# Optimization experiments

Hardware: AMD Instinct MI355X
Metric: run time of the kernel (lower is better)

Reference implementation:

```python
import jax, jax.numpy as jnp
import numpy as np

NEG_SLOPE_GAT = 0.2   # PyG GATConv default negative_slope
NEG_SLOPE = 0.01      # torch.nn.LeakyReLU default
NUM_AISLES = 20       # aisle_nrs drawn from [0,20); matches aisle_nrs.max()+1


def leaky(x, s):
    return jnp.where(x >= 0, x, s * x)


def gat_conv(x, src, dst, W, a_src, a_dst, b, n_nodes):
    """Single-head PyG GATConv (self-loops already appended to src/dst)."""
    h = x @ W                                        # [N, C]
    es = h @ a_src                                   # [N]
    ed = h @ a_dst                                   # [N]
    e = leaky(es[src] + ed[dst], NEG_SLOPE_GAT)      # [E] per-edge score
    m = jax.ops.segment_max(e, dst, num_segments=n_nodes)
    w = jnp.exp(e - m[dst])
    z = jax.ops.segment_sum(w, dst, num_segments=n_nodes)
    alpha = w / z[dst]                               # segment softmax over incoming edges
    out = jax.ops.segment_sum(h[src] * alpha[:, None], dst, num_segments=n_nodes)
    return out + b


def setup_inputs() -> dict:
    key = jax.random.key(0)
    ks = jax.random.split(key, 32)
    B, N, E = 16, 2048, 32768
    Fin, H, O, HA = 32, 128, 64, 256

    def glorot(k, shape):
        fan = shape[0] + shape[-1]
        return jax.random.uniform(k, shape, jnp.float32, -1.0, 1.0) * np.sqrt(6.0 / fan)

    inp = {
        "graph_nodes": jax.random.normal(ks[0], (B, N, Fin), jnp.float32),
        "aisle_nrs": jax.random.randint(ks[1], (B, N), 0, NUM_AISLES),
        "graph_edge_links": jax.random.randint(ks[2], (B, 2, E), 0, N),
        "mask": jax.random.randint(ks[3], (B, N), 0, 2),
        "picks_left": jax.random.randint(ks[4], (B,), 0, 100),
        # GAT layer 1: Fin -> H
        "W1": glorot(ks[5], (Fin, H)), "as1": glorot(ks[6], (H,)), "ad1": glorot(ks[7], (H,)), "b1": jnp.zeros((H,), jnp.float32),
        # GAT layer 2: H -> H
        "W2": glorot(ks[8], (H, H)), "as2": glorot(ks[9], (H,)), "ad2": glorot(ks[10], (H,)), "b2": jnp.zeros((H,), jnp.float32),
        # GAT layer 3: H -> O
        "W3": glorot(ks[11], (H, O)), "as3": glorot(ks[12], (O,)), "ad3": glorot(ks[13], (O,)), "b3": jnp.zeros((O,), jnp.float32),
        # post-embedding MLP head
        "lw1": glorot(ks[14], (2 * O, HA)), "lb1": jnp.zeros((HA,), jnp.float32),
        "lw2": glorot(ks[15], (HA, O)), "lb2": jnp.zeros((O,), jnp.float32),
        "lw3": glorot(ks[16], (O, 1)), "lb3": jnp.zeros((1,), jnp.float32),
    }
    return inp


def reference(graph_nodes, aisle_nrs, graph_edge_links, mask, picks_left,
              W1, as1, ad1, b1, W2, as2, ad2, b2, W3, as3, ad3, b3,
              lw1, lb1, lw2, lb2, lw3, lb3):
    B, N, Fin = graph_nodes.shape
    NT = B * N
    x = graph_nodes.reshape(NT, Fin)

    # batch the graphs: offset per-graph edge indices, append self-loops
    off = (jnp.arange(B) * N)[:, None]
    src = (graph_edge_links[:, 0, :] + off).reshape(-1)
    dst = (graph_edge_links[:, 1, :] + off).reshape(-1)
    loops = jnp.arange(NT)
    src = jnp.concatenate([src, loops])
    dst = jnp.concatenate([dst, loops])

    x = gat_conv(x, src, dst, W1, as1, ad1, b1, NT)
    x = gat_conv(x, src, dst, W2, as2, ad2, b2, NT)
    x = gat_conv(x, src, dst, W3, as3, ad3, b3, NT)

    # scatter-mean aisle embedding
    batch_idx = jnp.repeat(jnp.arange(B), N)
    aid = aisle_nrs.reshape(-1) + batch_idx * NUM_AISLES   # [NT]
    S = B * NUM_AISLES
    ssum = jax.ops.segment_sum(x, aid, num_segments=S)
    cnt = jax.ops.segment_sum(jnp.ones((NT,), x.dtype), aid, num_segments=S)
    emb = ssum / jnp.maximum(cnt, 1.0)[:, None]

    x = jnp.concatenate([x, emb[aid]], axis=1)             # [NT, 2*O]
    x = leaky(x @ lw1 + lb1, NEG_SLOPE)
    x = leaky(x @ lw2 + lb2, NEG_SLOPE)
    x = (x @ lw3 + lb3).reshape(B, N)

    logits = jnp.where(mask != 0, x, -jnp.inf)
    return jax.nn.softmax(logits, axis=1)
```

## Files before the change

### kernel.cpp

```cpp
#include <hip/hip_runtime.h>
#include <hip/hip_bf16.h>
#include <math.h>
#include <stdint.h>

#define BATCH 16
#define NNODE 2048
#define EPG   32768
#define NT    (BATCH * NNODE)
#define ET    (BATCH * EPG + NT)
#define NUM_AISLES 20
#define SEG   (BATCH * NUM_AISLES)
#define NEG_GAT 0.2f
#define NEG_MLP 0.01f
#define ACHUNK 8
#define CAP 64

typedef __attribute__((ext_vector_type(8))) short s16x8;
typedef __attribute__((ext_vector_type(4))) float f32x4;

__device__ __forceinline__ void split_bf16(float v, unsigned short& hi, unsigned short& lo) {
    unsigned int u = __float_as_uint(v);
    unsigned int r = u + 0x7FFFu + ((u >> 16) & 1u);
    hi = (unsigned short)(r >> 16);
    float fh = __uint_as_float(((unsigned int)hi) << 16);
    float rem = v - fh;
    unsigned int u2 = __float_as_uint(rem);
    unsigned int r2 = u2 + 0x7FFFu + ((u2 >> 16) & 1u);
    lo = (unsigned short)(r2 >> 16);
}

template <int K, int KC, int NOUT, int COLS>
__device__ __forceinline__ void prep_one(const float* __restrict__ W,
                                         unsigned short* __restrict__ dst, int idx) {
    constexpr int SWM = (KC >= 64) ? 7 : 3;
    int k = idx / NOUT, col = idx - k * NOUT;
    int ch = k / KC, kl = k - ch * KC;
    int ct = col / COLS, n = col - ct * COLS;
    int tile = ct * (K / KC) + ch;
    unsigned short h, l;
    split_bf16(W[idx], h, l);
    size_t base = (size_t)tile * (2 * COLS * KC);
    int pos = n * KC + (kl ^ ((n & SWM) << 3));
    dst[base + pos] = h;
    dst[base + COLS * KC + pos] = l;
}

__global__ __launch_bounds__(256) void prep_weights(const float* __restrict__ W1,
                                                    const float* __restrict__ W2,
                                                    const float* __restrict__ W3,
                                                    const float* __restrict__ lw1,
                                                    const float* __restrict__ lw2,
                                                    unsigned short* __restrict__ P1,
                                                    unsigned short* __restrict__ P2,
                                                    unsigned short* __restrict__ P3,
                                                    unsigned short* __restrict__ P4,
                                                    unsigned short* __restrict__ P5) {
    int b = blockIdx.x, t = threadIdx.x;
    if (b < 16)        prep_one<32, 32, 128, 128>(W1, P1, b * 256 + t);
    else if (b < 80)   prep_one<128, 64, 128, 128>(W2, P2, (b - 16) * 256 + t);
    else if (b < 112)  prep_one<128, 128, 64, 64>(W3, P3, (b - 80) * 256 + t);
    else if (b < 240)  prep_one<128, 64, 256, 128>(lw1, P4, (b - 112) * 256 + t);
    else               prep_one<256, 128, 64, 64>(lw2, P5, (b - 240) * 256 + t);
}

__global__ __launch_bounds__(256) void edge_scatter(const int* __restrict__ links,
                                                    int* __restrict__ cnt,
                                                    int* __restrict__ col_bkt) {
    int b = blockIdx.x;
    int s, d;
    if (b < 2048) {
        int xcd = b & 7, idx = b >> 3;
        int g = xcd * 2 + (idx >> 7);
        int chunk = idx & 127;
        int i = chunk * 256 + threadIdx.x;
        const int* pb = links + (size_t)g * 2 * EPG;
        s = pb[i] + (g << 11);
        d = pb[EPG + i] + (g << 11);
    } else {
        int b2 = b - 2048;
        int xcd = b2 & 7, idx = b2 >> 3;
        int g = xcd * 2 + (idx >> 3);
        int chunk = idx & 7;
        s = d = g * NNODE + chunk * 256 + threadIdx.x;
    }
    int pos = atomicAdd(&cnt[d], 1);
    if (pos < CAP) col_bkt[d * CAP + pos] = s;
}

template <int K, int KC, int NOUT, int COLS, bool LEAKY, bool ATTN, bool FINAL, bool CONCAT>
__global__ __launch_bounds__(256) void gemm_mfma(const float* __restrict__ A,
                                                 const unsigned short* __restrict__ WP,
                                                 const float* __restrict__ bias,
                                                 float* __restrict__ out,
                                                 const float* __restrict__ a_src,
                                                 const float* __restrict__ a_dst,
                                                 float* __restrict__ es,
                                                 float* __restrict__ ed,
                                                 const float* __restrict__ emb,
                                                 const int* __restrict__ aisle,
                                                 const float* __restrict__ lw3,
                                                 const float* __restrict__ lb3,
                                                 const int* __restrict__ mask,
                                                 float* __restrict__ logits) {
    constexpr int C = COLS / 16;
    constexpr int SWM = (KC >= 64) ? 7 : 3;
    constexpr int TILE_US = COLS * KC;
    constexpr int TB2 = 2 * TILE_US * 2;
    static_assert(TB2 % 4096 == 0, "chunk must be a multiple of one 256-thread 16B sweep");

    __shared__ unsigned short WS[2 * TILE_US];

    const int tid = threadIdx.x;
    const int wave = tid >> 6, lane = tid & 63;
    const int quad = lane >> 4, l15 = lane & 15;
    const int row0 = blockIdx.x * 64;
    const int m = row0 + wave * 16 + l15;

    f32x4 acc[C];
#pragma unroll
    for (int c = 0; c < C; ++c)
#pragma unroll
        for (int v = 0; v < 4; ++v) acc[c][v] = 0.f;

    union SU { s16x8 v; unsigned short u[8]; };

    for (int kb = 0; kb < K; kb += KC) {
        const char* gsrc = (const char*)WP
            + (size_t)(blockIdx.y * (K / KC) + kb / KC) * TB2;
#pragma unroll
        for (int s = 0; s < TB2 / 4096; ++s) {
            __builtin_amdgcn_global_load_lds(
                (const __attribute__((address_space(1))) void*)(gsrc + s * 4096 + wave * 1024 + lane * 16),
                (__attribute__((address_space(3))) void*)&WS[(s * 4096 + wave * 1024) >> 1],
                16, 0, 0);
        }
        __syncthreads();

        for (int kc = kb; kc < kb + KC; kc += 32) {
            const int off = kc + quad * 8;
            const float* srcp;
            if constexpr (CONCAT) {
                if (off < 64) {
                    srcp = A + (size_t)m * 64 + off;
                } else {
                    int g = m >> 11;
                    srcp = emb + ((size_t)(g * NUM_AISLES + aisle[m])) * 64 + (off - 64);
                }
            } else {
                srcp = A + (size_t)m * K + off;
            }
            float4 v0 = ((const float4*)srcp)[0];
            float4 v1 = ((const float4*)srcp)[1];
            float a8[8] = {v0.x, v0.y, v0.z, v0.w, v1.x, v1.y, v1.z, v1.w};
            SU ah, al;
#pragma unroll
            for (int j = 0; j < 8; ++j) split_bf16(a8[j], ah.u[j], al.u[j]);

            const int kq = (kc - kb) + quad * 8;
#pragma unroll
            for (int c = 0; c < C; ++c) {
                int n = c * 16 + l15;
                int pos = n * KC + (kq ^ ((n & SWM) << 3));
                s16x8 wh = *(const s16x8*)&WS[pos];
                s16x8 wl = *(const s16x8*)&WS[TILE_US + pos];
                acc[c] = __builtin_amdgcn_mfma_f32_16x16x32_bf16(ah.v, wh, acc[c], 0, 0, 0);
                acc[c] = __builtin_amdgcn_mfma_f32_16x16x32_bf16(ah.v, wl, acc[c], 0, 0, 0);
                acc[c] = __builtin_amdgcn_mfma_f32_16x16x32_bf16(al.v, wh, acc[c], 0, 0, 0);
            }
        }
        if (kb + KC < K) __syncthreads();
    }
    if constexpr (FINAL) {
#pragma unroll
        for (int reg = 0; reg < 4; ++reg) {
            float p = 0.f;
#pragma unroll
            for (int c = 0; c < C; ++c) {
                int colx = c * 16 + l15;
                float v = acc[c][reg] + bias[colx];
                v = v >= 0.f ? v : NEG_MLP * v;
                p += v * lw3[colx];
            }
#pragma unroll
            for (int mk = 1; mk < 16; mk <<= 1) p += __shfl_xor(p, mk, 64);
            if (l15 == 0) {
                int row = row0 + wave * 16 + quad * 4 + reg;
                float lg = p + lb3[0];
                logits[row] = (mask[row] != 0) ? lg : -INFINITY;
            }
        }
    } else {
#pragma unroll
        for (int c = 0; c < C; ++c) {
            int colx = blockIdx.y * COLS + c * 16 + l15;
            float bv = bias ? bias[colx] : 0.f;
#pragma unroll
            for (int reg = 0; reg < 4; ++reg) {
                int row = row0 + wave * 16 + quad * 4 + reg;
                float v = acc[c][reg] + bv;
                if (LEAKY) v = v >= 0.f ? v : NEG_MLP * v;
                out[(size_t)row * NOUT + colx] = v;
            }
        }
        if constexpr (ATTN) {
#pragma unroll
            for (int reg = 0; reg < 4; ++reg) {
                float ps = 0.f, pd = 0.f;
#pragma unroll
                for (int c = 0; c < C; ++c) {
                    int colx = c * 16 + l15;
                    float v = acc[c][reg];
                    ps += v * a_src[colx];
                    pd += v * a_dst[colx];
                }
#pragma unroll
                for (int mk = 1; mk < 16; mk <<= 1) {
                    ps += __shfl_xor(ps, mk, 64);
                    pd += __shfl_xor(pd, mk, 64);
                }
                if (l15 == 0) {
                    int row = row0 + wave * 16 + quad * 4 + reg;
                    es[row] = ps;
                    ed[row] = pd;
                }
            }
        }
    }
}

template <int HD>
__global__ __launch_bounds__(256) void gat_aggregate(const float* __restrict__ h,
                                                     const float* __restrict__ es,
                                                     const float* __restrict__ ed,
                                                     const int* __restrict__ cnt,
                                                     const int* __restrict__ col_bkt,
                                                     const float* __restrict__ bias,
                                                     float* __restrict__ out) {
    int b = blockIdx.x;
    int xcd = b & 7, q = b >> 3;
    int graph = xcd * 2 + (q >> 9);
    int node = graph * NNODE + (q & 511) * 4 + (threadIdx.x >> 6);
    int lane = threadIdx.x & 63;
    int deg = cnt[node];
    deg = deg < CAP ? deg : CAP;
    float edv = ed[node];

    float e0 = -INFINITY;
    int c0v = 0;
    if (lane < deg) {
        c0v = col_bkt[node * CAP + lane];
        float e = es[c0v] + edv;
        e0 = e >= 0.f ? e : NEG_GAT * e;
    }
    float m = e0;
#pragma unroll
    for (int off = 32; off; off >>= 1) m = fmaxf(m, __shfl_xor(m, off, 64));
    float z = __expf(e0 - m);
#pragma unroll
    for (int off = 32; off; off >>= 1) z += __shfl_xor(z, off, 64);
    float w0 = __expf(e0 - m) / z;

    const int quad = lane >> 4, l15 = lane & 15;
    if (HD == 128) {
        float a0 = 0.f, a1 = 0.f, a2 = 0.f, a3 = 0.f;
        float a4 = 0.f, a5 = 0.f, a6 = 0.f, a7 = 0.f;
        for (int jj = 0; jj < deg; jj += 4) {
            int j2 = jj + quad;
            int s = __shfl(c0v, j2, 64);
            float w = __shfl(w0, j2, 64);
            const float* base = h + (size_t)s * 128 + l15 * 8;
            float4 v0 = *(const float4*)base;
            float4 v1 = *(const float4*)(base + 4);
            a0 += w * v0.x; a1 += w * v0.y; a2 += w * v0.z; a3 += w * v0.w;
            a4 += w * v1.x; a5 += w * v1.y; a6 += w * v1.z; a7 += w * v1.w;
        }
#pragma unroll
        for (int off = 16; off <= 32; off <<= 1) {
            a0 += __shfl_xor(a0, off, 64); a1 += __shfl_xor(a1, off, 64);
            a2 += __shfl_xor(a2, off, 64); a3 += __shfl_xor(a3, off, 64);
            a4 += __shfl_xor(a4, off, 64); a5 += __shfl_xor(a5, off, 64);
            a6 += __shfl_xor(a6, off, 64); a7 += __shfl_xor(a7, off, 64);
        }
        if (quad == 0) {
            const float* bb = bias + l15 * 8;
            float4 o0, o1;
            o0.x = a0 + bb[0]; o0.y = a1 + bb[1]; o0.z = a2 + bb[2]; o0.w = a3 + bb[3];
            o1.x = a4 + bb[4]; o1.y = a5 + bb[5]; o1.z = a6 + bb[6]; o1.w = a7 + bb[7];
            float* op = out + (size_t)node * 128 + l15 * 8;
            *(float4*)op = o0;
            *(float4*)(op + 4) = o1;
        }
    } else {
        float a0 = 0.f, a1 = 0.f, a2 = 0.f, a3 = 0.f;
        for (int jj = 0; jj < deg; jj += 4) {
            int j2 = jj + quad;
            int s = __shfl(c0v, j2, 64);
            float w = __shfl(w0, j2, 64);
            float4 v = *(const float4*)(h + (size_t)s * 64 + l15 * 4);
            a0 += w * v.x; a1 += w * v.y; a2 += w * v.z; a3 += w * v.w;
        }
#pragma unroll
        for (int off = 16; off <= 32; off <<= 1) {
            a0 += __shfl_xor(a0, off, 64); a1 += __shfl_xor(a1, off, 64);
            a2 += __shfl_xor(a2, off, 64); a3 += __shfl_xor(a3, off, 64);
        }
        if (quad == 0) {
            const float* bb = bias + l15 * 4;
            float4 o;
            o.x = a0 + bb[0]; o.y = a1 + bb[1]; o.z = a2 + bb[2]; o.w = a3 + bb[3];
            *(float4*)(out + (size_t)node * 64 + l15 * 4) = o;
        }
    }
}

__global__ __launch_bounds__(256) void aisle_partial(const float* __restrict__ x3,
                                                     const int* __restrict__ aisle,
                                                     float* __restrict__ psum,
                                                     int* __restrict__ pcnt) {
    int g = blockIdx.x >> 3;
    int ch = blockIdx.x & 7;
    int f = threadIdx.x & 63;
    int stripe = threadIdx.x >> 6;

    __shared__ float sacc[4][NUM_AISLES][64];
    __shared__ int scnt[4][NUM_AISLES];
    for (int i = threadIdx.x; i < 4 * NUM_AISLES * 64; i += 256)
        ((float*)sacc)[i] = 0.f;
    for (int i = threadIdx.x; i < 4 * NUM_AISLES; i += 256)
        ((int*)scnt)[i] = 0;
    __syncthreads();

    const int* ai = aisle + g * NNODE;
    const float* xg = x3 + (size_t)g * NNODE * 64;
    int n0 = ch * 256 + stripe * 64;
#pragma unroll 4
    for (int i = 0; i < 64; ++i) {
        int n = n0 + i;
        int a = ai[n];
        float v = xg[(size_t)n * 64 + f];
        sacc[stripe][a][f] += v;
        if (f == 0) scnt[stripe][a]++;
    }
    __syncthreads();

    for (int i = threadIdx.x; i < NUM_AISLES * 64; i += 256) {
        int a = i >> 6, ff = i & 63;
        psum[((size_t)blockIdx.x * NUM_AISLES + a) * 64 + ff] =
            sacc[0][a][ff] + sacc[1][a][ff] + sacc[2][a][ff] + sacc[3][a][ff];
    }
    for (int i = threadIdx.x; i < NUM_AISLES; i += 256) {
        pcnt[blockIdx.x * NUM_AISLES + i] =
            scnt[0][i] + scnt[1][i] + scnt[2][i] + scnt[3][i];
    }
}

__global__ __launch_bounds__(256) void aisle_reduce(const float* __restrict__ psum,
                                                    const int* __restrict__ pcnt,
                                                    float* __restrict__ emb) {
    int idx = blockIdx.x * 256 + threadIdx.x;
    if (idx >= SEG * 64) return;
    int seg = idx >> 6;
    int f = idx & 63;
    int g = seg / NUM_AISLES;
    int a = seg - g * NUM_AISLES;
    float s = 0.f;
    int c = 0;
#pragma unroll
    for (int ch = 0; ch < ACHUNK; ++ch) {
        int blk = g * ACHUNK + ch;
        s += psum[((size_t)blk * NUM_AISLES + a) * 64 + f];
        c += pcnt[blk * NUM_AISLES + a];
    }
    emb[idx] = s / fmaxf((float)c, 1.0f);
}

__global__ __launch_bounds__(256) void softmax_kernel(const float* __restrict__ logits,
                                                      float* __restrict__ out) {
    int b = blockIdx.x;
    const float* lr = logits + b * NNODE;
    __shared__ float red[4], redz[4];
    float m = -INFINITY;
    for (int i = threadIdx.x; i < NNODE; i += 256) m = fmaxf(m, lr[i]);
#pragma unroll
    for (int off = 32; off; off >>= 1) m = fmaxf(m, __shfl_xor(m, off, 64));
    if ((threadIdx.x & 63) == 0) red[threadIdx.x >> 6] = m;
    __syncthreads();
    m = fmaxf(fmaxf(red[0], red[1]), fmaxf(red[2], red[3]));
    float z = 0.f;
    for (int i = threadIdx.x; i < NNODE; i += 256) z += __expf(lr[i] - m);
#pragma unroll
    for (int off = 32; off; off >>= 1) z += __shfl_xor(z, off, 64);
    if ((threadIdx.x & 63) == 0) redz[threadIdx.x >> 6] = z;
    __syncthreads();
    z = redz[0] + redz[1] + redz[2] + redz[3];
    float invz = 1.0f / z;
    for (int i = threadIdx.x; i < NNODE; i += 256) {
        float v = lr[i];
        out[b * NNODE + i] = (v == -INFINITY) ? 0.f : __expf(v - m) * invz;
    }
}


extern "C" void kernel_launch(void* const* d_in, const int* in_sizes, int n_in,
                              void* d_out, int out_size, void* d_ws, size_t ws_size,
                              hipStream_t stream) {
    const float* gn   = (const float*)d_in[0];
    const int* aisle  = (const int*)d_in[1];
    const int* links  = (const int*)d_in[2];
    const int* mask   = (const int*)d_in[3];
    const float* W1  = (const float*)d_in[5];
    const float* as1 = (const float*)d_in[6];
    const float* ad1 = (const float*)d_in[7];
    const float* b1  = (const float*)d_in[8];
    const float* W2  = (const float*)d_in[9];
    const float* as2 = (const float*)d_in[10];
    const float* ad2 = (const float*)d_in[11];
    const float* b2  = (const float*)d_in[12];
    const float* W3  = (const float*)d_in[13];
    const float* as3 = (const float*)d_in[14];
    const float* ad3 = (const float*)d_in[15];
    const float* b3  = (const float*)d_in[16];
    const float* lw1 = (const float*)d_in[17];
    const float* lb1 = (const float*)d_in[18];
    const float* lw2 = (const float*)d_in[19];
    const float* lb2 = (const float*)d_in[20];
    const float* lw3 = (const float*)d_in[21];
    const float* lb3 = (const float*)d_in[22];
    float* out = (float*)d_out;

    float* ws = (float*)d_ws;
    float* h      = ws;
    float* xb     = h + (size_t)NT * 128;
    float* es     = xb + (size_t)NT * 128;
    float* ed     = es + NT;
    float* emb    = ed + NT;
    float* y1     = emb + SEG * 64;
    float* y2     = y1 + (size_t)NT * 256;
    float* logits = y2 + (size_t)NT * 64;
    float* psum   = logits + NT;
    int* pcnt     = (int*)(psum + 128 * NUM_AISLES * 64);
    int* row_ptr  = pcnt + 128 * NUM_AISLES;
    int* cnt      = row_ptr + NT + 1;
    int* col_bkt  = (int*)y2;

    unsigned short* wsplit = (unsigned short*)(((uintptr_t)(cnt + NT) + 255) & ~(uintptr_t)255);
    unsigned short* P1 = wsplit;
    unsigned short* P2 = P1 + 8192;
    unsigned short* P3 = P2 + 32768;
    unsigned short* P4 = P3 + 16384;
    unsigned short* P5 = P4 + 65536;

    const int EB = (ET + 255) / 256;

    hipMemsetAsync(cnt, 0, NT * sizeof(int), stream);
    prep_weights<<<304, 256, 0, stream>>>(W1, W2, W3, lw1, lw2, P1, P2, P3, P4, P5);
    edge_scatter<<<EB, 256, 0, stream>>>(links, cnt, col_bkt);

    gemm_mfma<32, 32, 128, 128, false, true, false, false><<<dim3(NT / 64, 1), 256, 0, stream>>>(
        gn, P1, nullptr, h, as1, ad1, es, ed, nullptr, nullptr, nullptr, nullptr, nullptr, nullptr);
    gat_aggregate<128><<<NT / 4, 256, 0, stream>>>(h, es, ed, cnt, col_bkt, b1, xb);

    gemm_mfma<128, 64, 128, 128, false, true, false, false><<<dim3(NT / 64, 1), 256, 0, stream>>>(
        xb, P2, nullptr, h, as2, ad2, es, ed, nullptr, nullptr, nullptr, nullptr, nullptr, nullptr);
    gat_aggregate<128><<<NT / 4, 256, 0, stream>>>(h, es, ed, cnt, col_bkt, b2, xb);

    gemm_mfma<128, 128, 64, 64, false, true, false, false><<<dim3(NT / 64, 1), 256, 0, stream>>>(
        xb, P3, nullptr, h, as3, ad3, es, ed, nullptr, nullptr, nullptr, nullptr, nullptr, nullptr);
    gat_aggregate<64><<<NT / 4, 256, 0, stream>>>(h, es, ed, cnt, col_bkt, b3, xb);

    aisle_partial<<<BATCH * ACHUNK, 256, 0, stream>>>(xb, aisle, psum, pcnt);
    aisle_reduce<<<(SEG * 64 + 255) / 256, 256, 0, stream>>>(psum, pcnt, emb);

    gemm_mfma<128, 64, 256, 128, true, false, false, true><<<dim3(NT / 64, 2), 256, 0, stream>>>(
        xb, P4, lb1, y1, nullptr, nullptr, nullptr, nullptr, emb, aisle, nullptr, nullptr, nullptr, nullptr);
    gemm_mfma<256, 128, 64, 64, true, false, true, false><<<dim3(NT / 64, 1), 256, 0, stream>>>(
        y1, P5, lb2, y2, nullptr, nullptr, nullptr, nullptr, nullptr, nullptr, lw3, lb3, mask, logits);

    softmax_kernel<<<BATCH, 256, 0, stream>>>(logits, out);
}
```

Baseline: 284.8 us.

## Fuse launches and store activations pre-split as packed bf16 hi/lo pairs

Folds the counter memset into the weight-prep kernel, merges edge scatter with the first GEMM launch, and computes the aisle mean inside the concat GEMM via shared memory instead of a separate reduce kernel. Aggregation and MLP outputs are now stored as packed hi/lo bf16 words, so consuming GEMMs skip the per-element split in their inner loop. This cuts launch count and redundant conversion ALU work. In exchange, the packed representation drops some low mantissa bits, and every concat block recomputes the aisle embedding.

Result: faster. 277.0 us (-2.8%).

```diff
diff --git a/kernel.cpp b/kernel.cpp
--- a/kernel.cpp
+++ b/kernel.cpp
@@ -14,6 +14,7 @@
 #define NEG_MLP 0.01f
 #define ACHUNK 8
 #define CAP 64
+#define EMB_LD 72
 
 typedef __attribute__((ext_vector_type(8))) short s16x8;
 typedef __attribute__((ext_vector_type(4))) float f32x4;
@@ -27,6 +28,16 @@
     unsigned int u2 = __float_as_uint(rem);
     unsigned int r2 = u2 + 0x7FFFu + ((u2 >> 16) & 1u);
     lo = (unsigned short)(r2 >> 16);
+}
+
+__device__ __forceinline__ unsigned int pack_bf16(float v) {
+    unsigned short h, l;
+    split_bf16(v, h, l);
+    return ((unsigned int)h << 16) | l;
+}
+
+__device__ __forceinline__ float unpack_f32(unsigned int u) {
+    return __uint_as_float(u & 0xffff0000u) + __uint_as_float(u << 16);
 }
 
 template <int K, int KC, int NOUT, int COLS>
@@ -54,19 +65,20 @@
                                                     unsigned short* __restrict__ P2,
                                                     unsigned short* __restrict__ P3,
                                                     unsigned short* __restrict__ P4,
-                                                    unsigned short* __restrict__ P5) {
+                                                    unsigned short* __restrict__ P5,
+                                                    int* __restrict__ cnt) {
     int b = blockIdx.x, t = threadIdx.x;
     if (b < 16)        prep_one<32, 32, 128, 128>(W1, P1, b * 256 + t);
     else if (b < 80)   prep_one<128, 64, 128, 128>(W2, P2, (b - 16) * 256 + t);
     else if (b < 112)  prep_one<128, 128, 64, 64>(W3, P3, (b - 80) * 256 + t);
     else if (b < 240)  prep_one<128, 64, 256, 128>(lw1, P4, (b - 112) * 256 + t);
-    else               prep_one<256, 128, 64, 64>(lw2, P5, (b - 240) * 256 + t);
-}
-
-__global__ __launch_bounds__(256) void edge_scatter(const int* __restrict__ links,
-                                                    int* __restrict__ cnt,
-                                                    int* __restrict__ col_bkt) {
-    int b = blockIdx.x;
+    else if (b < 304)  prep_one<256, 128, 64, 64>(lw2, P5, (b - 240) * 256 + t);
+    else               cnt[(b - 304) * 256 + t] = 0;
+}
+
+__device__ __forceinline__ void scatter_body(int b, const int* __restrict__ links,
+                                             int* __restrict__ cnt,
+                                             int* __restrict__ col_bkt) {
     int s, d;
     if (b < 2048) {
         int xcd = b & 7, idx = b >> 3;
@@ -87,21 +99,24 @@
     if (pos < CAP) col_bkt[d * CAP + pos] = s;
 }
 
-template <int K, int KC, int NOUT, int COLS, bool LEAKY, bool ATTN, bool FINAL, bool CONCAT>
-__global__ __launch_bounds__(256) void gemm_mfma(const float* __restrict__ A,
-                                                 const unsigned short* __restrict__ WP,
-                                                 const float* __restrict__ bias,
-                                                 float* __restrict__ out,
-                                                 const float* __restrict__ a_src,
-                                                 const float* __restrict__ a_dst,
-                                                 float* __restrict__ es,
-                                                 float* __restrict__ ed,
-                                                 const float* __restrict__ emb,
-                                                 const int* __restrict__ aisle,
-                                                 const float* __restrict__ lw3,
-                                                 const float* __restrict__ lb3,
-                                                 const int* __restrict__ mask,
-                                                 float* __restrict__ logits) {
+template <int K, int KC, int NOUT, int COLS, bool LEAKY, bool ATTN, bool FINAL,
+          bool CONCAT, bool PACKEDA, bool PACKOUT>
+__device__ __forceinline__ void gemm_body(int bx, int by,
+                                          const void* __restrict__ Aptr,
+                                          const unsigned short* __restrict__ WP,
+                                          const float* __restrict__ bias,
+                                          void* __restrict__ outp,
+                                          const float* __restrict__ a_src,
+                                          const float* __restrict__ a_dst,
+                                          float* __restrict__ es,
+                                          float* __restrict__ ed,
+                                          const float* __restrict__ psum,
+                                          const int* __restrict__ pcnt,
+                                          const int* __restrict__ aisle,
+                                          const float* __restrict__ lw3,
+                                          const float* __restrict__ lb3,
+                                          const int* __restrict__ mask,
+                                          float* __restrict__ logits) {
     constexpr int C = COLS / 16;
     constexpr int SWM = (KC >= 64) ? 7 : 3;
     constexpr int TILE_US = COLS * KC;
@@ -109,12 +124,30 @@
     static_assert(TB2 % 4096 == 0, "chunk must be a multiple of one 256-thread 16B sweep");
 
     __shared__ unsigned short WS[2 * TILE_US];
+    __shared__ float emb_s[CONCAT ? NUM_AISLES * EMB_LD : 1];
 
     const int tid = threadIdx.x;
     const int wave = tid >> 6, lane = tid & 63;
     const int quad = lane >> 4, l15 = lane & 15;
-    const int row0 = blockIdx.x * 64;
+    const int row0 = bx * 64;
     const int m = row0 + wave * 16 + l15;
+
+    int am = 0;
+    if constexpr (CONCAT) {
+        int g = row0 >> 11;
+        for (int i = tid; i < NUM_AISLES * 64; i += 256) {
+            int a = i >> 6, f = i & 63;
+            float s = 0.f;
+            int c = 0;
+#pragma unroll
+            for (int ch = 0; ch < ACHUNK; ++ch) {
+                s += psum[((size_t)(g * ACHUNK + ch) * NUM_AISLES + a) * 64 + f];
+                c += pcnt[(g * ACHUNK + ch) * NUM_AISLES + a];
+            }
+            emb_s[a * EMB_LD + f] = s / fmaxf((float)c, 1.0f);
+        }
+        am = aisle[m];
+    }
 
     f32x4 acc[C];
 #pragma unroll
@@ -126,7 +159,7 @@
 
     for (int kb = 0; kb < K; kb += KC) {
         const char* gsrc = (const char*)WP
-            + (size_t)(blockIdx.y * (K / KC) + kb / KC) * TB2;
+            + (size_t)(by * (K / KC) + kb / KC) * TB2;
 #pragma unroll
         for (int s = 0; s < TB2 / 4096; ++s) {
             __builtin_amdgcn_global_load_lds(
@@ -138,23 +171,44 @@
 
         for (int kc = kb; kc < kb + KC; kc += 32) {
             const int off = kc + quad * 8;
-            const float* srcp;
+            SU ah, al;
             if constexpr (CONCAT) {
                 if (off < 64) {
-                    srcp = A + (size_t)m * 64 + off;
+                    const unsigned int* ap = (const unsigned int*)Aptr + (size_t)m * 64 + off;
+                    uint4 u0 = ((const uint4*)ap)[0];
+                    uint4 u1 = ((const uint4*)ap)[1];
+                    unsigned int uu[8] = {u0.x, u0.y, u0.z, u0.w, u1.x, u1.y, u1.z, u1.w};
+#pragma unroll
+                    for (int j = 0; j < 8; ++j) {
+                        ah.u[j] = (unsigned short)(uu[j] >> 16);
+                        al.u[j] = (unsigned short)uu[j];
+                    }
                 } else {
-                    int g = m >> 11;
-                    srcp = emb + ((size_t)(g * NUM_AISLES + aisle[m])) * 64 + (off - 64);
+                    const float* ep = &emb_s[am * EMB_LD + (off - 64)];
+                    float4 v0 = ((const float4*)ep)[0];
+                    float4 v1 = ((const float4*)ep)[1];
+                    float a8[8] = {v0.x, v0.y, v0.z, v0.w, v1.x, v1.y, v1.z, v1.w};
+#pragma unroll
+                    for (int j = 0; j < 8; ++j) split_bf16(a8[j], ah.u[j], al.u[j]);
+                }
+            } else if constexpr (PACKEDA) {
+                const unsigned int* ap = (const unsigned int*)Aptr + (size_t)m * K + off;
+                uint4 u0 = ((const uint4*)ap)[0];
+                uint4 u1 = ((const uint4*)ap)[1];
+                unsigned int uu[8] = {u0.x, u0.y, u0.z, u0.w, u1.x, u1.y, u1.z, u1.w};
+#pragma unroll
+                for (int j = 0; j < 8; ++j) {
+                    ah.u[j] = (unsigned short)(uu[j] >> 16);
+                    al.u[j] = (unsigned short)uu[j];
                 }
             } else {
-                srcp = A + (size_t)m * K + off;
-            }
-            float4 v0 = ((const float4*)srcp)[0];
-            float4 v1 = ((const float4*)srcp)[1];
-            float a8[8] = {v0.x, v0.y, v0.z, v0.w, v1.x, v1.y, v1.z, v1.w};
-            SU ah, al;
-#pragma unroll
-            for (int j = 0; j < 8; ++j) split_bf16(a8[j], ah.u[j], al.u[j]);
+                const float* srcp = (const float*)Aptr + (size_t)m * K + off;
+                float4 v0 = ((const float4*)srcp)[0];
+                float4 v1 = ((const float4*)srcp)[1];
+                float a8[8] = {v0.x, v0.y, v0.z, v0.w, v1.x, v1.y, v1.z, v1.w};
+#pragma unroll
+                for (int j = 0; j < 8; ++j) split_bf16(a8[j], ah.u[j], al.u[j]);
+            }
 
             const int kq = (kc - kb) + quad * 8;
 #pragma unroll
@@ -192,14 +246,18 @@
     } else {
 #pragma unroll
         for (int c = 0; c < C; ++c) {
-            int colx = blockIdx.y * COLS + c * 16 + l15;
+            int colx = by * COLS + c * 16 + l15;
             float bv = bias ? bias[colx] : 0.f;
 #pragma unroll
             for (int reg = 0; reg < 4; ++reg) {
                 int row = row0 + wave * 16 + quad * 4 + reg;
                 float v = acc[c][reg] + bv;
                 if (LEAKY) v = v >= 0.f ? v : NEG_MLP * v;
-                out[(size_t)row * NOUT + colx] = v;
+                if constexpr (PACKOUT) {
+                    ((unsigned int*)outp)[(size_t)row * NOUT + colx] = pack_bf16(v);
+                } else {
+                    ((float*)outp)[(size_t)row * NOUT + colx] = v;
+                }
             }
         }
         if constexpr (ATTN) {
@@ -228,6 +286,47 @@
     }
 }
 
+template <int K, int KC, int NOUT, int COLS, bool LEAKY, bool ATTN, bool FINAL,
+          bool CONCAT, bool PACKEDA, bool PACKOUT>
+__global__ __launch_bounds__(256) void gemm_mfma(const void* __restrict__ A,
+                                                 const unsigned short* __restrict__ WP,
+                                                 const float* __restrict__ bias,
+                                                 void* __restrict__ out,
+                                                 const float* __restrict__ a_src,
+                                                 const float* __restrict__ a_dst,
+                                                 float* __restrict__ es,
+                                                 float* __restrict__ ed,
+                                                 const float* __restrict__ psum,
+                                                 const int* __restrict__ pcnt,
+                                                 const int* __restrict__ aisle,
+                                                 const float* __restrict__ lw3,
+                                                 const float* __restrict__ lb3,
+                                                 const int* __restrict__ mask,
+                                                 float* __restrict__ logits) {
+    gemm_body<K, KC, NOUT, COLS, LEAKY, ATTN, FINAL, CONCAT, PACKEDA, PACKOUT>(
+        blockIdx.x, blockIdx.y, A, WP, bias, out, a_src, a_dst, es, ed,
+        psum, pcnt, aisle, lw3, lb3, mask, logits);
+}
+
+__global__ __launch_bounds__(256) void gemm1_scatter(const float* __restrict__ A,
+                                                     const unsigned short* __restrict__ WP,
+                                                     float* __restrict__ out,
+                                                     const float* __restrict__ a_src,
+                                                     const float* __restrict__ a_dst,
+                                                     float* __restrict__ es,
+                                                     float* __restrict__ ed,
+                                                     const int* __restrict__ links,
+                                                     int* __restrict__ cnt,
+                                                     int* __restrict__ col_bkt) {
+    if (blockIdx.x >= NT / 64) {
+        scatter_body(blockIdx.x - NT / 64, links, cnt, col_bkt);
+        return;
+    }
+    gemm_body<32, 32, 128, 128, false, true, false, false, false, false>(
+        blockIdx.x, 0, A, WP, nullptr, out, a_src, a_dst, es, ed,
+        nullptr, nullptr, nullptr, nullptr, nullptr, nullptr, nullptr);
+}
+
 template <int HD>
 __global__ __launch_bounds__(256) void gat_aggregate(const float* __restrict__ h,
                                                      const float* __restrict__ es,
@@ -235,7 +334,7 @@
                                                      const int* __restrict__ cnt,
                                                      const int* __restrict__ col_bkt,
                                                      const float* __restrict__ bias,
-                                                     float* __restrict__ out) {
+                                                     unsigned int* __restrict__ out) {
     int b = blockIdx.x;
     int xcd = b & 7, q = b >> 3;
     int graph = xcd * 2 + (q >> 9);
@@ -283,12 +382,14 @@
         }
         if (quad == 0) {
             const float* bb = bias + l15 * 8;
-            float4 o0, o1;
-            o0.x = a0 + bb[0]; o0.y = a1 + bb[1]; o0.z = a2 + bb[2]; o0.w = a3 + bb[3];
-            o1.x = a4 + bb[4]; o1.y = a5 + bb[5]; o1.z = a6 + bb[6]; o1.w = a7 + bb[7];
-            float* op = out + (size_t)node * 128 + l15 * 8;
-            *(float4*)op = o0;
-            *(float4*)(op + 4) = o1;
+            uint4 p0, p1;
+            p0.x = pack_bf16(a0 + bb[0]); p0.y = pack_bf16(a1 + bb[1]);
+            p0.z = pack_bf16(a2 + bb[2]); p0.w = pack_bf16(a3 + bb[3]);
+            p1.x = pack_bf16(a4 + bb[4]); p1.y = pack_bf16(a5 + bb[5]);
+            p1.z = pack_bf16(a6 + bb[6]); p1.w = pack_bf16(a7 + bb[7]);
+            unsigned int* op = out + (size_t)node * 128 + l15 * 8;
+            *(uint4*)op = p0;
+            *(uint4*)(op + 4) = p1;
         }
     } else {
         float a0 = 0.f, a1 = 0.f, a2 = 0.f, a3 = 0.f;
@@ -306,14 +407,15 @@
         }
         if (quad == 0) {
             const float* bb = bias + l15 * 4;
-            float4 o;
-            o.x = a0 + bb[0]; o.y = a1 + bb[1]; o.z = a2 + bb[2]; o.w = a3 + bb[3];
-            *(float4*)(out + (size_t)node * 64 + l15 * 4) = o;
-        }
-    }
-}
-
-__global__ __launch_bounds__(256) void aisle_partial(const float* __restrict__ x3,
+            uint4 p;
+            p.x = pack_bf16(a0 + bb[0]); p.y = pack_bf16(a1 + bb[1]);
+            p.z = pack_bf16(a2 + bb[2]); p.w = pack_bf16(a3 + bb[3]);
+            *(uint4*)(out + (size_t)node * 64 + l15 * 4) = p;
+        }
+    }
+}
+
+__global__ __launch_bounds__(256) void aisle_partial(const unsigned int* __restrict__ x3,
                                                      const int* __restrict__ aisle,
                                                      float* __restrict__ psum,
                                                      int* __restrict__ pcnt) {
@@ -331,13 +433,13 @@
     __syncthreads();
 
     const int* ai = aisle + g * NNODE;
-    const float* xg = x3 + (size_t)g * NNODE * 64;
+    const unsigned int* xg = x3 + (size_t)g * NNODE * 64;
     int n0 = ch * 256 + stripe * 64;
 #pragma unroll 4
     for (int i = 0; i < 64; ++i) {
         int n = n0 + i;
         int a = ai[n];
-        float v = xg[(size_t)n * 64 + f];
+        float v = unpack_f32(xg[(size_t)n * 64 + f]);
         sacc[stripe][a][f] += v;
         if (f == 0) scnt[stripe][a]++;
     }
@@ -352,26 +454,6 @@
         pcnt[blockIdx.x * NUM_AISLES + i] =
             scnt[0][i] + scnt[1][i] + scnt[2][i] + scnt[3][i];
     }
-}
-
-__global__ __launch_bounds__(256) void aisle_reduce(const float* __restrict__ psum,
-                                                    const int* __restrict__ pcnt,
-                                                    float* __restrict__ emb) {
-    int idx = blockIdx.x * 256 + threadIdx.x;
-    if (idx >= SEG * 64) return;
-    int seg = idx >> 6;
-    int f = idx & 63;
-    int g = seg / NUM_AISLES;
-    int a = seg - g * NUM_AISLES;
-    float s = 0.f;
-    int c = 0;
-#pragma unroll
-    for (int ch = 0; ch < ACHUNK; ++ch) {
-        int blk = g * ACHUNK + ch;
-        s += psum[((size_t)blk * NUM_AISLES + a) * 64 + f];
-        c += pcnt[blk * NUM_AISLES + a];
-    }
-    emb[idx] = s / fmaxf((float)c, 1.0f);
 }
 
 __global__ __launch_bounds__(256) void softmax_kernel(const float* __restrict__ logits,
@@ -452,29 +534,27 @@
 
     const int EB = (ET + 255) / 256;
 
-    hipMemsetAsync(cnt, 0, NT * sizeof(int), stream);
-    prep_weights<<<304, 256, 0, stream>>>(W1, W2, W3, lw1, lw2, P1, P2, P3, P4, P5);
-    edge_scatter<<<EB, 256, 0, stream>>>(links, cnt, col_bkt);
-
-    gemm_mfma<32, 32, 128, 128, false, true, false, false><<<dim3(NT / 64, 1), 256, 0, stream>>>(
-        gn, P1, nullptr, h, as1, ad1, es, ed, nullptr, nullptr, nullptr, nullptr, nullptr, nullptr);
-    gat_aggregate<128><<<NT / 4, 256, 0, stream>>>(h, es, ed, cnt, col_bkt, b1, xb);
-
-    gemm_mfma<128, 64, 128, 128, false, true, false, false><<<dim3(NT / 64, 1), 256, 0, stream>>>(
-        xb, P2, nullptr, h, as2, ad2, es, ed, nullptr, nullptr, nullptr, nullptr, nullptr, nullptr);
-    gat_aggregate<128><<<NT / 4, 256, 0, stream>>>(h, es, ed, cnt, col_bkt, b2, xb);
-
-    gemm_mfma<128, 128, 64, 64, false, true, false, false><<<dim3(NT / 64, 1), 256, 0, stream>>>(
-        xb, P3, nullptr, h, as3, ad3, es, ed, nullptr, nullptr, nullptr, nullptr, nullptr, nullptr);
-    gat_aggregate<64><<<NT / 4, 256, 0, stream>>>(h, es, ed, cnt, col_bkt, b3, xb);
-
-    aisle_partial<<<BATCH * ACHUNK, 256, 0, stream>>>(xb, aisle, psum, pcnt);
-    aisle_reduce<<<(SEG * 64 + 255) / 256, 256, 0, stream>>>(psum, pcnt, emb);
-
-    gemm_mfma<128, 64, 256, 128, true, false, false, true><<<dim3(NT / 64, 2), 256, 0, stream>>>(
-        xb, P4, lb1, y1, nullptr, nullptr, nullptr, nullptr, emb, aisle, nullptr, nullptr, nullptr, nullptr);
-    gemm_mfma<256, 128, 64, 64, true, false, true, false><<<dim3(NT / 64, 1), 256, 0, stream>>>(
-        y1, P5, lb2, y2, nullptr, nullptr, nullptr, nullptr, nullptr, nullptr, lw3, lb3, mask, logits);
+    prep_weights<<<432, 256, 0, stream>>>(W1, W2, W3, lw1, lw2, P1, P2, P3, P4, P5, cnt);
+
+    gemm1_scatter<<<NT / 64 + EB, 256, 0, stream>>>(gn, P1, h, as1, ad1, es, ed,
+                                                    links, cnt, col_bkt);
+    gat_aggregate<128><<<NT / 4, 256, 0, stream>>>(h, es, ed, cnt, col_bkt, b1, (unsigned int*)xb);
+
+    gemm_mfma<128, 64, 128, 128, false, true, false, false, true, false><<<dim3(NT / 64, 1), 256, 0, stream>>>(
+        xb, P2, nullptr, h, as2, ad2, es, ed, nullptr, nullptr, nullptr, nullptr, nullptr, nullptr, nullptr);
+    gat_aggregate<128><<<NT / 4, 256, 0, stream>>>(h, es, ed, cnt, col_bkt, b2, (unsigned int*)xb);
+
+    gemm_mfma<128, 128, 64, 64, false, true, false, false, true, false><<<dim3(NT / 64, 1), 256, 0, stream>>>(
+        xb, P3, nullptr, h, as3, ad3, es, ed, nullptr, nullptr, nullptr, nullptr, nullptr, nullptr, nullptr);
+    gat_aggregate<64><<<NT / 4, 256, 0, stream>>>(h, es, ed, cnt, col_bkt, b3, (unsigned int*)xb);
+
+    aisle_partial<<<BATCH * ACHUNK, 256, 0, stream>>>((const unsigned int*)xb, aisle, psum, pcnt);
+
+    gemm_mfma<128, 64, 256, 128, true, false, false, true, false, true><<<dim3(NT / 64, 2), 256, 0, stream>>>(
+        xb, P4, lb1, y1, nullptr, nullptr, nullptr, nullptr, psum, pcnt, aisle, nullptr, nullptr, nullptr, nullptr);
+
+    gemm_mfma<256, 128, 64, 64, true, false, true, false, true, false><<<dim3(NT / 64, 1), 256, 0, stream>>>(
+        y1, P5, lb2, nullptr, nullptr, nullptr, nullptr, nullptr, nullptr, nullptr, nullptr, lw3, lb3, mask, logits);
 
     softmax_kernel<<<BATCH, 256, 0, stream>>>(logits, out);
 }
```
